# Kernel optimization log

Measured on AMD Instinct MI355X. Metric: run time of the kernel, lower is better.

Reference implementation:

```python
import jax, jax.numpy as jnp
import numpy as np

N_NODES = 100000
N_EDGES = 1600000


def setup_inputs() -> dict:
    key = jax.random.key(0)
    ks = jax.random.split(key, 5)
    x = jax.random.normal(ks[0], (N_NODES, 128), dtype=jnp.float32)
    edge_index = jax.random.randint(ks[1], (2, N_EDGES), 0, N_NODES, dtype=jnp.int64)
    edge_weight = jnp.ones((N_EDGES,), dtype=jnp.float32)
    W1 = jax.random.normal(ks[2], (128, 128), dtype=jnp.float32) * (1.0 / np.sqrt(128))
    b1 = jnp.zeros((128,), dtype=jnp.float32)
    W2 = jax.random.normal(ks[3], (128, 64), dtype=jnp.float32) * (1.0 / np.sqrt(128))
    b2 = jnp.zeros((64,), dtype=jnp.float32)
    return {"x": x, "edge_index": edge_index, "edge_weight": edge_weight,
            "W1": W1, "b1": b1, "W2": W2, "b2": b2}


def _gcn_conv(x, rows, cols, W, b, n_nodes):
    # GCNConv(normalize=True), unit edge weights (forward overwrites weights with ones)
    h = x @ W                                             # [N, out]
    ones_w = jnp.ones(rows.shape[0], dtype=x.dtype)
    deg = jax.ops.segment_sum(ones_w, cols, num_segments=n_nodes)   # in-degree at targets
    dinv = jnp.where(deg > 0, deg ** -0.5, 0.0)
    norm = dinv[rows] * dinv[cols]                        # [E+N]
    msg = h[rows] * norm[:, None]                         # gather + scale, memory-bound
    out = jax.ops.segment_sum(msg, cols, num_segments=n_nodes)
    return out + b


def reference(x, edge_index, edge_weight, W1, b1, W2, b2):
    n = x.shape[0]
    loop = jnp.arange(n, dtype=edge_index.dtype)
    rows = jnp.concatenate([edge_index[0], loop])         # self-loops (PyG default)
    cols = jnp.concatenate([edge_index[1], loop])
    h = jax.nn.relu(_gcn_conv(x, rows, cols, W1, b1, n))
    logits = _gcn_conv(h, rows, cols, W2, b2, n)
    return logits
```

## Files before the change

### kernel.cpp

```cpp
#include <hip/hip_runtime.h>
#include <hip/hip_fp16.h>


constexpr int NN = 100000;
constexpr int NE = 1600000;
constexpr int BSH = 7;
constexpr int NB = (NN + 127) >> BSH;
constexpr int NBLK = 256;
constexpr int EPB = NE / NBLK;
constexpr int TSTR = 784;

typedef _Float16 f16x8 __attribute__((ext_vector_type(8)));
typedef float f32x4 __attribute__((ext_vector_type(4)));

__global__ __launch_bounds__(256) void k_histwt(const int* __restrict__ cols,
                                                int* __restrict__ table,
                                                const float* __restrict__ W1,
                                                const float* __restrict__ W2,
                                                __half* __restrict__ Wt1,
                                                __half* __restrict__ Wt2) {
  if (blockIdx.x < NBLK) {
    __shared__ int cnt[NB];
    for (int i = threadIdx.x; i < NB; i += 256) cnt[i] = 0;
    __syncthreads();
    int base = blockIdx.x * EPB;
    for (int i = threadIdx.x; i < EPB; i += 256)
      atomicAdd(&cnt[cols[base + i] >> BSH], 1);
    __syncthreads();
    for (int i = threadIdx.x; i < NB; i += 256)
      table[blockIdx.x * TSTR + i] = cnt[i];
  } else {
    int i = (blockIdx.x - NBLK) * 256 + threadIdx.x;
    if (i < 16384) {
      int k = i >> 7, n = i & 127;
      Wt1[n * 128 + k] = __float2half(W1[i]);
    } else {
      int j = i - 16384;
      int k = j >> 6, n = j & 63;
      Wt2[n * 128 + k] = __float2half(W2[j]);
    }
  }
}

__global__ __launch_bounds__(256) void k_scanT(const int* __restrict__ table,
                                               int* __restrict__ startOff,
                                               int* __restrict__ btot) {
  __shared__ int s[256];
  int b = blockIdx.x, t = threadIdx.x;
  int v = table[t * TSTR + b];
  s[t] = v;
  __syncthreads();
  for (int off = 1; off < 256; off <<= 1) {
    int tmp = (t >= off) ? s[t - off] : 0;
    __syncthreads();
    s[t] += tmp;
    __syncthreads();
  }
  startOff[t * TSTR + b] = s[t] - v;
  if (t == 255) btot[b] = s[t];
}

__global__ __launch_bounds__(256) void k_scatB(const int* __restrict__ rows,
                                               const int* __restrict__ cols,
                                               const int* __restrict__ startOff,
                                               const int* __restrict__ btot,
                                               int* __restrict__ bucketBase,
                                               unsigned* __restrict__ binned) {
  __shared__ int bb[NB];
  __shared__ int s[256];
  __shared__ int scnt[NB];
  int tid = threadIdx.x;
  int base4 = tid * 4;
  int d0 = (base4 + 0 < NB) ? btot[base4 + 0] : 0;
  int d1 = (base4 + 1 < NB) ? btot[base4 + 1] : 0;
  int d2 = (base4 + 2 < NB) ? btot[base4 + 2] : 0;
  int d3 = (base4 + 3 < NB) ? btot[base4 + 3] : 0;
  int tsum = d0 + d1 + d2 + d3;
  s[tid] = tsum;
  __syncthreads();
  for (int off = 1; off < 256; off <<= 1) {
    int tmp = (tid >= off) ? s[tid - off] : 0;
    __syncthreads();
    s[tid] += tmp;
    __syncthreads();
  }
  int ex = s[tid] - tsum;
  if (base4 + 0 < NB) bb[base4 + 0] = ex;
  if (base4 + 1 < NB) bb[base4 + 1] = ex + d0;
  if (base4 + 2 < NB) bb[base4 + 2] = ex + d0 + d1;
  if (base4 + 3 < NB) bb[base4 + 3] = ex + d0 + d1 + d2;
  __syncthreads();
  if (blockIdx.x == 0)
    for (int i = tid; i < NB; i += 256) bucketBase[i] = bb[i];
  for (int i = tid; i < NB; i += 256)
    scnt[i] = bb[i] + startOff[blockIdx.x * TSTR + i];
  __syncthreads();
  int base = blockIdx.x * EPB;
  for (int i = tid; i < EPB; i += 256) {
    int c = cols[base + i];
    int r = rows[base + i];
    int pos = atomicAdd(&scnt[c >> BSH], 1);
    binned[pos] = ((unsigned)r << BSH) | (unsigned)(c & 127);
  }
}

__global__ __launch_bounds__(256) void k_fillb(const unsigned* __restrict__ binned,
                                               const int* __restrict__ bucketBase,
                                               const int* __restrict__ btot,
                                               int* __restrict__ rowptr,
                                               int* __restrict__ deg,
                                               float* __restrict__ dinv,
                                               int* __restrict__ srcIdx,
                                               const float4* __restrict__ x4,
                                               float2* __restrict__ y8) {
  __shared__ int cnt[128];
  __shared__ int sc[128];
  __shared__ int rp[128];
  __shared__ float sdv[128];
  int b = blockIdx.x;
  int nb0 = b << BSH;
  int nn = min(128, NN - nb0);
  int tid = threadIdx.x;
  if (tid < 128) cnt[tid] = 0;
  __syncthreads();
  int ebeg = bucketBase[b];
  int eend = ebeg + btot[b];
  for (int p = ebeg + tid; p < eend; p += 256)
    atomicAdd(&cnt[binned[p] & 127], 1);
  __syncthreads();
  int v = (tid < 128) ? cnt[tid] : 0;
  if (tid < 128) sc[tid] = v;
  __syncthreads();
  for (int off = 1; off < 128; off <<= 1) {
    int tmp = (tid < 128 && tid >= off) ? sc[tid - off] : 0;
    __syncthreads();
    if (tid < 128) sc[tid] += tmp;
    __syncthreads();
  }
  if (tid < 128) {
    int ex = sc[tid] - v;
    rp[tid] = ebeg + ex;
    float dv = rsqrtf((float)v + 1.0f);
    sdv[tid] = dv;
    if (tid < nn) {
      rowptr[nb0 + tid] = ebeg + ex;
      deg[nb0 + tid] = v;
      dinv[nb0 + tid] = dv;
    }
    cnt[tid] = 0;
  }
  __syncthreads();
  for (int p = ebeg + tid; p < eend; p += 256) {
    unsigned pk = binned[p];
    int cl = pk & 127;
    int local = atomicAdd(&cnt[cl], 1);
    srcIdx[rp[cl] + local] = (int)(pk >> BSH);
  }
  int tot = nn << 5;
  const float4* xb = x4 + ((size_t)nb0 << 5);
  float2* yb = y8 + ((size_t)nb0 << 5);
  for (int i = tid; i < tot; i += 256) {
    float sfac = sdv[i >> 5];
    float4 vv = xb[i];
    union { __half2 h[2]; float2 f; } u;
    u.h[0] = __floats2half2_rn(vv.x * sfac, vv.y * sfac);
    u.h[1] = __floats2half2_rn(vv.z * sfac, vv.w * sfac);
    yb[i] = u.f;
  }
}

__global__ __launch_bounds__(256, 8) void k_fused(
    const __half* __restrict__ y, const int* __restrict__ rowptr,
    const int* __restrict__ deg, const int* __restrict__ srcIdx,
    const float* __restrict__ dinv, const __half* __restrict__ Wt1,
    const float* __restrict__ b1, const __half* __restrict__ Wt2,
    __half* __restrict__ z) {
  __shared__ __align__(16) __half sA[16][136];
  __shared__ __align__(16) __half sB[16][136];
  const int w = threadIdx.x >> 6, l = threadIdx.x & 63;
  const int blk0 = blockIdx.x * 16;
  const int quad = l >> 4, m = l & 15;

  for (int i = 0; i < 4; ++i) {
    const int lr = w * 4 + i;
    const int node = blk0 + lr;
    const int d = deg[node];
    const int ptr = rowptr[node];
    float acc[8];
#pragma unroll
    for (int j = 0; j < 8; j++) acc[j] = 0.0f;
    for (int base = 0; base < d; base += 64) {
      int cnt = min(64, d - base);
      int my = (l < cnt) ? srcIdx[ptr + base + l] : 0;
      int k = 0;
      for (; k + 16 <= cnt; k += 16) {
        int s0 = __shfl(my, k + quad);
        int s1 = __shfl(my, k + 4 + quad);
        int s2 = __shfl(my, k + 8 + quad);
        int s3 = __shfl(my, k + 12 + quad);
        f16x8 v0 = *reinterpret_cast<const f16x8*>(y + (size_t)s0 * 128 + m * 8);
        f16x8 v1 = *reinterpret_cast<const f16x8*>(y + (size_t)s1 * 128 + m * 8);
        f16x8 v2 = *reinterpret_cast<const f16x8*>(y + (size_t)s2 * 128 + m * 8);
        f16x8 v3 = *reinterpret_cast<const f16x8*>(y + (size_t)s3 * 128 + m * 8);
#pragma unroll
        for (int j = 0; j < 8; j++) acc[j] += (float)v0[j];
#pragma unroll
        for (int j = 0; j < 8; j++) acc[j] += (float)v1[j];
#pragma unroll
        for (int j = 0; j < 8; j++) acc[j] += (float)v2[j];
#pragma unroll
        for (int j = 0; j < 8; j++) acc[j] += (float)v3[j];
      }
      for (; k + 8 <= cnt; k += 8) {
        int s0 = __shfl(my, k + quad);
        int s1 = __shfl(my, k + 4 + quad);
        f16x8 v0 = *reinterpret_cast<const f16x8*>(y + (size_t)s0 * 128 + m * 8);
        f16x8 v1 = *reinterpret_cast<const f16x8*>(y + (size_t)s1 * 128 + m * 8);
#pragma unroll
        for (int j = 0; j < 8; j++) acc[j] += (float)v0[j];
#pragma unroll
        for (int j = 0; j < 8; j++) acc[j] += (float)v1[j];
      }
      for (; k < cnt; k += 4) {
        int idx = k + quad;
        bool valid = idx < cnt;
        int s0 = __shfl(my, valid ? idx : 0);
        f16x8 v0 = *reinterpret_cast<const f16x8*>(y + (size_t)s0 * 128 + m * 8);
        if (valid) {
#pragma unroll
          for (int j = 0; j < 8; j++) acc[j] += (float)v0[j];
        }
      }
    }
#pragma unroll
    for (int j = 0; j < 8; j++) acc[j] += __shfl_xor(acc[j], 16);
#pragma unroll
    for (int j = 0; j < 8; j++) acc[j] += __shfl_xor(acc[j], 32);
    if (quad == 0) {
      f16x8 sv = *reinterpret_cast<const f16x8*>(y + (size_t)node * 128 + m * 8);
      float scn = dinv[node];
      f16x8 o;
#pragma unroll
      for (int j = 0; j < 8; j++)
        o[j] = (_Float16)((acc[j] + (float)sv[j]) * scn);
      *reinterpret_cast<f16x8*>(&sA[lr][m * 8]) = o;
    }
  }
  __syncthreads();

  f16x8 afrag[4];
#pragma unroll
  for (int kk = 0; kk < 4; kk++)
    afrag[kk] = *reinterpret_cast<const f16x8*>(&sA[m][kk * 32 + quad * 8]);
  f32x4 acc1[2];
#pragma unroll
  for (int t = 0; t < 2; t++) {
    float bv = b1[(w * 2 + t) * 16 + m];
    acc1[t] = (f32x4){bv, bv, bv, bv};
  }
#pragma unroll
  for (int kk = 0; kk < 4; kk++) {
#pragma unroll
    for (int t = 0; t < 2; t++) {
      f16x8 b = *reinterpret_cast<const f16x8*>(
          Wt1 + (size_t)((w * 2 + t) * 16 + m) * 128 + kk * 32 + quad * 8);
      acc1[t] = __builtin_amdgcn_mfma_f32_16x16x32_f16(afrag[kk], b, acc1[t], 0, 0, 0);
    }
  }
#pragma unroll
  for (int t = 0; t < 2; t++)
#pragma unroll
    for (int i = 0; i < 4; i++)
      sB[quad * 4 + i][(w * 2 + t) * 16 + m] =
          __float2half(fmaxf(acc1[t][i], 0.0f));
  __syncthreads();

  f16x8 hfrag[4];
#pragma unroll
  for (int kk = 0; kk < 4; kk++)
    hfrag[kk] = *reinterpret_cast<const f16x8*>(&sB[m][kk * 32 + quad * 8]);
  f32x4 acc2 = (f32x4){0.f, 0.f, 0.f, 0.f};
#pragma unroll
  for (int kk = 0; kk < 4; kk++) {
    f16x8 b = *reinterpret_cast<const f16x8*>(
        Wt2 + (size_t)(w * 16 + m) * 128 + kk * 32 + quad * 8);
    acc2 = __builtin_amdgcn_mfma_f32_16x16x32_f16(hfrag[kk], b, acc2, 0, 0, 0);
  }
  float rs[4];
#pragma unroll
  for (int i = 0; i < 4; i++) rs[i] = dinv[blk0 + quad * 4 + i];
#pragma unroll
  for (int i = 0; i < 4; i++)
    sA[quad * 4 + i][w * 16 + m] = __float2half(acc2[i] * rs[i]);
  __syncthreads();

  if (threadIdx.x < 128) {
    int r = threadIdx.x >> 3, cc = threadIdx.x & 7;
    *reinterpret_cast<float4*>(z + (size_t)(blk0 + r) * 64 + cc * 8) =
        *reinterpret_cast<const float4*>(&sA[r][cc * 8]);
  }
}

__global__ __launch_bounds__(256) void k_gath2(const __half* __restrict__ z,
                                               const int* __restrict__ rowptr,
                                               const int* __restrict__ deg,
                                               const int* __restrict__ srcIdx,
                                               const float* __restrict__ dinv,
                                               const float* __restrict__ b2,
                                               float* __restrict__ out) {
  int node = blockIdx.x * 4 + (threadIdx.x >> 6);
  if (node >= NN) return;
  int lane = threadIdx.x & 63;
  int g = lane >> 3;
  int c = lane & 7;
  int d = deg[node];
  int p = rowptr[node];
  size_t coff = (size_t)c * 8;
  float acc[8];
#pragma unroll
  for (int i = 0; i < 8; i++) acc[i] = 0.0f;

  for (int base = 0; base < d; base += 64) {
    int cnt = min(64, d - base);
    int my = (lane < cnt) ? srcIdx[p + base + lane] : 0;
    int k = 0;
    for (; k + 32 <= cnt; k += 32) {
      int s0 = __shfl(my, k + g);
      int s1 = __shfl(my, k + 8 + g);
      int s2 = __shfl(my, k + 16 + g);
      int s3 = __shfl(my, k + 24 + g);
      f16x8 v0 = *reinterpret_cast<const f16x8*>(z + (size_t)s0 * 64 + coff);
      f16x8 v1 = *reinterpret_cast<const f16x8*>(z + (size_t)s1 * 64 + coff);
      f16x8 v2 = *reinterpret_cast<const f16x8*>(z + (size_t)s2 * 64 + coff);
      f16x8 v3 = *reinterpret_cast<const f16x8*>(z + (size_t)s3 * 64 + coff);
#pragma unroll
      for (int i = 0; i < 8; i++) acc[i] += (float)v0[i];
#pragma unroll
      for (int i = 0; i < 8; i++) acc[i] += (float)v1[i];
#pragma unroll
      for (int i = 0; i < 8; i++) acc[i] += (float)v2[i];
#pragma unroll
      for (int i = 0; i < 8; i++) acc[i] += (float)v3[i];
    }
    for (; k + 16 <= cnt; k += 16) {
      int s0 = __shfl(my, k + g);
      int s1 = __shfl(my, k + 8 + g);
      f16x8 v0 = *reinterpret_cast<const f16x8*>(z + (size_t)s0 * 64 + coff);
      f16x8 v1 = *reinterpret_cast<const f16x8*>(z + (size_t)s1 * 64 + coff);
#pragma unroll
      for (int i = 0; i < 8; i++) acc[i] += (float)v0[i];
#pragma unroll
      for (int i = 0; i < 8; i++) acc[i] += (float)v1[i];
    }
    for (; k < cnt; k += 8) {
      int idx = k + g;
      bool valid = idx < cnt;
      int s0 = __shfl(my, valid ? idx : 0);
      f16x8 v0 = *reinterpret_cast<const f16x8*>(z + (size_t)s0 * 64 + coff);
      if (valid) {
#pragma unroll
        for (int i = 0; i < 8; i++) acc[i] += (float)v0[i];
      }
    }
  }
#pragma unroll
  for (int i = 0; i < 8; i++) acc[i] += __shfl_xor(acc[i], 8);
#pragma unroll
  for (int i = 0; i < 8; i++) acc[i] += __shfl_xor(acc[i], 16);
#pragma unroll
  for (int i = 0; i < 8; i++) acc[i] += __shfl_xor(acc[i], 32);
  if (g == 0) {
    f16x8 sv = *reinterpret_cast<const f16x8*>(z + (size_t)node * 64 + coff);
    float s = dinv[node];
    const float4* b4 = reinterpret_cast<const float4*>(b2);
    float4 bv0 = b4[2 * c], bv1 = b4[2 * c + 1];
    float4 o0, o1;
    o0.x = (acc[0] + (float)sv[0]) * s + bv0.x;
    o0.y = (acc[1] + (float)sv[1]) * s + bv0.y;
    o0.z = (acc[2] + (float)sv[2]) * s + bv0.z;
    o0.w = (acc[3] + (float)sv[3]) * s + bv0.w;
    o1.x = (acc[4] + (float)sv[4]) * s + bv1.x;
    o1.y = (acc[5] + (float)sv[5]) * s + bv1.y;
    o1.z = (acc[6] + (float)sv[6]) * s + bv1.z;
    o1.w = (acc[7] + (float)sv[7]) * s + bv1.w;
    float4* op = reinterpret_cast<float4*>(out + (size_t)node * 64 + coff);
    op[0] = o0;
    op[1] = o1;
  }
}

extern "C" void kernel_launch(void* const* d_in, const int* in_sizes, int n_in,
                              void* d_out, int out_size, void* d_ws, size_t ws_size,
                              hipStream_t stream) {
  const float* x  = (const float*)d_in[0];
  const int*   ei = (const int*)d_in[1];
  const int* rows = ei;
  const int* cols = ei + NE;
  const float* W1 = (const float*)d_in[3];
  const float* b1 = (const float*)d_in[4];
  const float* W2 = (const float*)d_in[5];
  const float* b2 = (const float*)d_in[6];
  float* out = (float*)d_out;

  char* base = (char*)d_ws;
  constexpr size_t MB = 1 << 20;
  int*      deg       = (int*)(base + 0 * MB);
  int*      rowptr    = (int*)(base + 1 * MB);
  float*    dinv      = (float*)(base + 2 * MB);
  int*      btot      = (int*)(base + 3 * MB);
  int*      bucketBase= (int*)(base + 3 * MB + 16 * 1024);
  __half*   Wt1       = (__half*)(base + 3 * MB + 64 * 1024);
  __half*   Wt2       = (__half*)(base + 3 * MB + 128 * 1024);
  int*      table     = (int*)(base + 4 * MB);
  int*      startOff  = (int*)(base + 5 * MB);
  unsigned* binned    = (unsigned*)(base + 6 * MB);
  int*      srcIdx    = (int*)(base + 13 * MB);
  __half*   y         = (__half*)(base + 20 * MB);
  __half*   z         = (__half*)(base + 46 * MB);

  k_histwt<<<NBLK + 96, 256, 0, stream>>>(cols, table, W1, W2, Wt1, Wt2);
  k_scanT<<<NB, 256, 0, stream>>>(table, startOff, btot);
  k_scatB<<<NBLK, 256, 0, stream>>>(rows, cols, startOff, btot, bucketBase,
                                    binned);
  k_fillb<<<NB, 256, 0, stream>>>(binned, bucketBase, btot, rowptr, deg, dinv,
                                  srcIdx, (const float4*)x, (float2*)y);
  k_fused<<<NN / 16, 256, 0, stream>>>(y, rowptr, deg, srcIdx, dinv,
                                       Wt1, b1, Wt2, z);
  k_gath2<<<(NN + 3) / 4, 256, 0, stream>>>(z, rowptr, deg, srcIdx, dinv, b2, out);
}
```

Before: 294.5 us.

## Split fused gather+GEMM kernel into separate gather and per-wave GEMM kernels

Replaces the fused layer-1 kernel, which gathered 16 nodes per block and then ran both MFMA GEMMs with block-wide syncs, with two kernels. The first is a one-node-per-wave gather that writes the aggregated fp16 features to a new buffer. The second is a GEMM kernel in which each wave handles 16 rows independently, with no block barriers. This is meant to improve gather occupancy and load balance and to remove the serialization between the gather and GEMM phases. The cost is an extra round trip of the 100000x128 fp16 intermediate through global memory and one more kernel launch. The 32-wide unrolled loop in the layer-2 gather is also removed.

```diff
diff --git a/kernel.cpp b/kernel.cpp
--- a/kernel.cpp
+++ b/kernel.cpp
@@ -169,135 +169,133 @@
   }
 }
 
-__global__ __launch_bounds__(256, 8) void k_fused(
-    const __half* __restrict__ y, const int* __restrict__ rowptr,
-    const int* __restrict__ deg, const int* __restrict__ srcIdx,
-    const float* __restrict__ dinv, const __half* __restrict__ Wt1,
+__global__ __launch_bounds__(256) void k_gath1(const __half* __restrict__ y,
+                                               const int* __restrict__ rowptr,
+                                               const int* __restrict__ deg,
+                                               const int* __restrict__ srcIdx,
+                                               const float* __restrict__ dinv,
+                                               __half* __restrict__ agg) {
+  int node = blockIdx.x * 4 + (threadIdx.x >> 6);
+  if (node >= NN) return;
+  int lane = threadIdx.x & 63;
+  int g = lane >> 4;
+  int c = lane & 15;
+  int d = deg[node];
+  int p = rowptr[node];
+  size_t coff = (size_t)c * 8;
+  float acc[8];
+#pragma unroll
+  for (int i = 0; i < 8; i++) acc[i] = 0.0f;
+
+  for (int base = 0; base < d; base += 64) {
+    int cnt = min(64, d - base);
+    int my = (lane < cnt) ? srcIdx[p + base + lane] : 0;
+    int k = 0;
+    for (; k + 8 <= cnt; k += 8) {
+      int s0 = __shfl(my, k + g);
+      int s1 = __shfl(my, k + 4 + g);
+      f16x8 v0 = *reinterpret_cast<const f16x8*>(y + (size_t)s0 * 128 + coff);
+      f16x8 v1 = *reinterpret_cast<const f16x8*>(y + (size_t)s1 * 128 + coff);
+#pragma unroll
+      for (int i = 0; i < 8; i++) acc[i] += (float)v0[i];
+#pragma unroll
+      for (int i = 0; i < 8; i++) acc[i] += (float)v1[i];
+    }
+    for (; k < cnt; k += 4) {
+      int idx = k + g;
+      bool valid = idx < cnt;
+      int s0 = __shfl(my, valid ? idx : 0);
+      f16x8 v0 = *reinterpret_cast<const f16x8*>(y + (size_t)s0 * 128 + coff);
+      if (valid) {
+#pragma unroll
+        for (int i = 0; i < 8; i++) acc[i] += (float)v0[i];
+      }
+    }
+  }
+#pragma unroll
+  for (int i = 0; i < 8; i++) acc[i] += __shfl_xor(acc[i], 16);
+#pragma unroll
+  for (int i = 0; i < 8; i++) acc[i] += __shfl_xor(acc[i], 32);
+  if (g == 0) {
+    f16x8 sv = *reinterpret_cast<const f16x8*>(y + (size_t)node * 128 + coff);
+    float sc = dinv[node];
+    union { __half2 h[4]; float4 f; } o;
+#pragma unroll
+    for (int j = 0; j < 4; j++) {
+      float a = (acc[2 * j]     + (float)sv[2 * j])     * sc;
+      float b = (acc[2 * j + 1] + (float)sv[2 * j + 1]) * sc;
+      o.h[j] = __floats2half2_rn(a, b);
+    }
+    *reinterpret_cast<float4*>(agg + (size_t)node * 128 + coff) = o.f;
+  }
+}
+
+__global__ __launch_bounds__(256, 4) void k_gemm12(
+    const __half* __restrict__ A, const __half* __restrict__ Wt1,
     const float* __restrict__ b1, const __half* __restrict__ Wt2,
-    __half* __restrict__ z) {
-  __shared__ __align__(16) __half sA[16][136];
-  __shared__ __align__(16) __half sB[16][136];
+    const float* __restrict__ dinv, __half* __restrict__ z) {
+  __shared__ __align__(16) __half sH[4][16][136];
   const int w = threadIdx.x >> 6, l = threadIdx.x & 63;
-  const int blk0 = blockIdx.x * 16;
   const int quad = l >> 4, m = l & 15;
-
-  for (int i = 0; i < 4; ++i) {
-    const int lr = w * 4 + i;
-    const int node = blk0 + lr;
-    const int d = deg[node];
-    const int ptr = rowptr[node];
-    float acc[8];
-#pragma unroll
-    for (int j = 0; j < 8; j++) acc[j] = 0.0f;
-    for (int base = 0; base < d; base += 64) {
-      int cnt = min(64, d - base);
-      int my = (l < cnt) ? srcIdx[ptr + base + l] : 0;
-      int k = 0;
-      for (; k + 16 <= cnt; k += 16) {
-        int s0 = __shfl(my, k + quad);
-        int s1 = __shfl(my, k + 4 + quad);
-        int s2 = __shfl(my, k + 8 + quad);
-        int s3 = __shfl(my, k + 12 + quad);
-        f16x8 v0 = *reinterpret_cast<const f16x8*>(y + (size_t)s0 * 128 + m * 8);
-        f16x8 v1 = *reinterpret_cast<const f16x8*>(y + (size_t)s1 * 128 + m * 8);
-        f16x8 v2 = *reinterpret_cast<const f16x8*>(y + (size_t)s2 * 128 + m * 8);
-        f16x8 v3 = *reinterpret_cast<const f16x8*>(y + (size_t)s3 * 128 + m * 8);
-#pragma unroll
-        for (int j = 0; j < 8; j++) acc[j] += (float)v0[j];
-#pragma unroll
-        for (int j = 0; j < 8; j++) acc[j] += (float)v1[j];
-#pragma unroll
-        for (int j = 0; j < 8; j++) acc[j] += (float)v2[j];
-#pragma unroll
-        for (int j = 0; j < 8; j++) acc[j] += (float)v3[j];
-      }
-      for (; k + 8 <= cnt; k += 8) {
-        int s0 = __shfl(my, k + quad);
-        int s1 = __shfl(my, k + 4 + quad);
-        f16x8 v0 = *reinterpret_cast<const f16x8*>(y + (size_t)s0 * 128 + m * 8);
-        f16x8 v1 = *reinterpret_cast<const f16x8*>(y + (size_t)s1 * 128 + m * 8);
-#pragma unroll
-        for (int j = 0; j < 8; j++) acc[j] += (float)v0[j];
-#pragma unroll
-        for (int j = 0; j < 8; j++) acc[j] += (float)v1[j];
-      }
-      for (; k < cnt; k += 4) {
-        int idx = k + quad;
-        bool valid = idx < cnt;
-        int s0 = __shfl(my, valid ? idx : 0);
-        f16x8 v0 = *reinterpret_cast<const f16x8*>(y + (size_t)s0 * 128 + m * 8);
-        if (valid) {
-#pragma unroll
-          for (int j = 0; j < 8; j++) acc[j] += (float)v0[j];
-        }
-      }
-    }
-#pragma unroll
-    for (int j = 0; j < 8; j++) acc[j] += __shfl_xor(acc[j], 16);
-#pragma unroll
-    for (int j = 0; j < 8; j++) acc[j] += __shfl_xor(acc[j], 32);
-    if (quad == 0) {
-      f16x8 sv = *reinterpret_cast<const f16x8*>(y + (size_t)node * 128 + m * 8);
-      float scn = dinv[node];
-      f16x8 o;
-#pragma unroll
-      for (int j = 0; j < 8; j++)
-        o[j] = (_Float16)((acc[j] + (float)sv[j]) * scn);
-      *reinterpret_cast<f16x8*>(&sA[lr][m * 8]) = o;
-    }
-  }
-  __syncthreads();
-
-  f16x8 afrag[4];
+  const int rowTop = blockIdx.x * 64 + w * 16;
+  if (rowTop >= NN) return;
+
+  int arow = rowTop + m;
+  const __half* ap = A + (size_t)arow * 128 + quad * 8;
+
+  f32x4 acc1[8];
+#pragma unroll
+  for (int t = 0; t < 8; t++) {
+    float bv = b1[t * 16 + m];
+    acc1[t] = (f32x4){bv, bv, bv, bv};
+  }
+#pragma unroll
+  for (int kc = 0; kc < 128; kc += 32) {
+    f16x8 a = *reinterpret_cast<const f16x8*>(ap + kc);
+#pragma unroll
+    for (int t = 0; t < 8; t++) {
+      f16x8 b = *reinterpret_cast<const f16x8*>(
+          Wt1 + (size_t)(t * 16 + m) * 128 + kc + quad * 8);
+      acc1[t] = __builtin_amdgcn_mfma_f32_16x16x32_f16(a, b, acc1[t], 0, 0, 0);
+    }
+  }
+#pragma unroll
+  for (int t = 0; t < 8; t++)
+#pragma unroll
+    for (int i = 0; i < 4; i++)
+      sH[w][quad * 4 + i][t * 16 + m] = __float2half(fmaxf(acc1[t][i], 0.0f));
+
+  f16x8 hfrag[4];
 #pragma unroll
   for (int kk = 0; kk < 4; kk++)
-    afrag[kk] = *reinterpret_cast<const f16x8*>(&sA[m][kk * 32 + quad * 8]);
-  f32x4 acc1[2];
-#pragma unroll
-  for (int t = 0; t < 2; t++) {
-    float bv = b1[(w * 2 + t) * 16 + m];
-    acc1[t] = (f32x4){bv, bv, bv, bv};
-  }
+    hfrag[kk] = *reinterpret_cast<const f16x8*>(&sH[w][m][kk * 32 + quad * 8]);
+  f32x4 acc2[4];
+#pragma unroll
+  for (int t = 0; t < 4; t++) acc2[t] = (f32x4){0.f, 0.f, 0.f, 0.f};
 #pragma unroll
   for (int kk = 0; kk < 4; kk++) {
 #pragma unroll
-    for (int t = 0; t < 2; t++) {
+    for (int t = 0; t < 4; t++) {
       f16x8 b = *reinterpret_cast<const f16x8*>(
-          Wt1 + (size_t)((w * 2 + t) * 16 + m) * 128 + kk * 32 + quad * 8);
-      acc1[t] = __builtin_amdgcn_mfma_f32_16x16x32_f16(afrag[kk], b, acc1[t], 0, 0, 0);
-    }
-  }
-#pragma unroll
-  for (int t = 0; t < 2; t++)
+          Wt2 + (size_t)(t * 16 + m) * 128 + kk * 32 + quad * 8);
+      acc2[t] = __builtin_amdgcn_mfma_f32_16x16x32_f16(hfrag[kk], b, acc2[t], 0, 0, 0);
+    }
+  }
+  float rs[4];
+#pragma unroll
+  for (int i = 0; i < 4; i++) rs[i] = dinv[rowTop + quad * 4 + i];
+#pragma unroll
+  for (int t = 0; t < 4; t++)
 #pragma unroll
     for (int i = 0; i < 4; i++)
-      sB[quad * 4 + i][(w * 2 + t) * 16 + m] =
-          __float2half(fmaxf(acc1[t][i], 0.0f));
-  __syncthreads();
-
-  f16x8 hfrag[4];
-#pragma unroll
-  for (int kk = 0; kk < 4; kk++)
-    hfrag[kk] = *reinterpret_cast<const f16x8*>(&sB[m][kk * 32 + quad * 8]);
-  f32x4 acc2 = (f32x4){0.f, 0.f, 0.f, 0.f};
-#pragma unroll
-  for (int kk = 0; kk < 4; kk++) {
-    f16x8 b = *reinterpret_cast<const f16x8*>(
-        Wt2 + (size_t)(w * 16 + m) * 128 + kk * 32 + quad * 8);
-    acc2 = __builtin_amdgcn_mfma_f32_16x16x32_f16(hfrag[kk], b, acc2, 0, 0, 0);
-  }
-  float rs[4];
-#pragma unroll
-  for (int i = 0; i < 4; i++) rs[i] = dinv[blk0 + quad * 4 + i];
-#pragma unroll
-  for (int i = 0; i < 4; i++)
-    sA[quad * 4 + i][w * 16 + m] = __float2half(acc2[i] * rs[i]);
-  __syncthreads();
-
-  if (threadIdx.x < 128) {
-    int r = threadIdx.x >> 3, cc = threadIdx.x & 7;
-    *reinterpret_cast<float4*>(z + (size_t)(blk0 + r) * 64 + cc * 8) =
-        *reinterpret_cast<const float4*>(&sA[r][cc * 8]);
+      sH[w][quad * 4 + i][t * 16 + m] = __float2half(acc2[t][i] * rs[i]);
+
+#pragma unroll
+  for (int rep = 0; rep < 2; rep++) {
+    int idx = rep * 64 + l;
+    int r = idx >> 3, cc = idx & 7;
+    *reinterpret_cast<float4*>(z + (size_t)(rowTop + r) * 64 + cc * 8) =
+        *reinterpret_cast<const float4*>(&sH[w][r][cc * 8]);
   }
 }
 
@@ -324,24 +322,6 @@
     int cnt = min(64, d - base);
     int my = (lane < cnt) ? srcIdx[p + base + lane] : 0;
     int k = 0;
-    for (; k + 32 <= cnt; k += 32) {
-      int s0 = __shfl(my, k + g);
-      int s1 = __shfl(my, k + 8 + g);
-      int s2 = __shfl(my, k + 16 + g);
-      int s3 = __shfl(my, k + 24 + g);
-      f16x8 v0 = *reinterpret_cast<const f16x8*>(z + (size_t)s0 * 64 + coff);
-      f16x8 v1 = *reinterpret_cast<const f16x8*>(z + (size_t)s1 * 64 + coff);
-      f16x8 v2 = *reinterpret_cast<const f16x8*>(z + (size_t)s2 * 64 + coff);
-      f16x8 v3 = *reinterpret_cast<const f16x8*>(z + (size_t)s3 * 64 + coff);
-#pragma unroll
-      for (int i = 0; i < 8; i++) acc[i] += (float)v0[i];
-#pragma unroll
-      for (int i = 0; i < 8; i++) acc[i] += (float)v1[i];
-#pragma unroll
-      for (int i = 0; i < 8; i++) acc[i] += (float)v2[i];
-#pragma unroll
-      for (int i = 0; i < 8; i++) acc[i] += (float)v3[i];
-    }
     for (; k + 16 <= cnt; k += 16) {
       int s0 = __shfl(my, k + g);
       int s1 = __shfl(my, k + 8 + g);
@@ -416,7 +396,8 @@
   unsigned* binned    = (unsigned*)(base + 6 * MB);
   int*      srcIdx    = (int*)(base + 13 * MB);
   __half*   y         = (__half*)(base + 20 * MB);
-  __half*   z         = (__half*)(base + 46 * MB);
+  __half*   aggx      = (__half*)(base + 46 * MB);
+  __half*   z         = (__half*)(base + 72 * MB);
 
   k_histwt<<<NBLK + 96, 256, 0, stream>>>(cols, table, W1, W2, Wt1, Wt2);
   k_scanT<<<NB, 256, 0, stream>>>(table, startOff, btot);
@@ -424,7 +405,7 @@
                                     binned);
   k_fillb<<<NB, 256, 0, stream>>>(binned, bucketBase, btot, rowptr, deg, dinv,
                                   srcIdx, (const float4*)x, (float2*)y);
-  k_fused<<<NN / 16, 256, 0, stream>>>(y, rowptr, deg, srcIdx, dinv,
-                                       Wt1, b1, Wt2, z);
+  k_gath1<<<(NN + 3) / 4, 256, 0, stream>>>(y, rowptr, deg, srcIdx, dinv, aggx);
+  k_gemm12<<<(NN + 63) / 64, 256, 0, stream>>>(aggx, Wt1, b1, Wt2, dinv, z);
   k_gath2<<<(NN + 3) / 4, 256, 0, stream>>>(z, rowptr, deg, srcIdx, dinv, b2, out);
 }
```

New measurement: 318.9 us. 8.3% more time.
